# Performance work log

Measured on AMD Instinct MI355X. Metric: run time of the kernel, lower is better.

## Reference

```python
import jax, jax.numpy as jnp
import numpy as np

N = 4096   # atoms
B = 64     # structures in batch
K = 128    # k-vectors per structure
E = 256    # emb_size_atom
D = 8      # downprojection_size
NUM_HIDDEN = 3


def _silu(x):
    return x * jax.nn.sigmoid(x)


def _residual(x, W):
    # ResidualLayer: two bias-free Dense(E,E) with SiLU, plus skip
    y = _silu(x @ W[0].T)
    y = _silu(y @ W[1].T)
    return x + y


def setup_inputs() -> dict:
    key = jax.random.key(0)
    ks = jax.random.split(key, 10)
    h = jax.random.normal(ks[0], (N, E), jnp.float32)
    x = jax.random.uniform(ks[1], (N, 3), jnp.float32) * 10.0  # Angstrom-scale positions
    k = jax.random.normal(ks[2], (B, K, 3), jnp.float32)
    batch_seg = jnp.sort(jax.random.randint(ks[3], (N,), 0, B))
    sc = 1.0 / np.sqrt(E)
    W_pre = jax.random.normal(ks[4], (2, E, E), jnp.float32) * sc        # pre_residual
    W_down = jax.random.normal(ks[5], (D, K), jnp.float32) / np.sqrt(K)  # shared downprojection (D,K)
    W_up = jax.random.normal(ks[6], (E, D), jnp.float32) / np.sqrt(D)    # up (E,D)
    W0 = jax.random.normal(ks[7], (E, E), jnp.float32) * sc              # first dense of ewald_layers
    W_res = jax.random.normal(ks[8], (NUM_HIDDEN, 2, E, E), jnp.float32) * sc
    return {"h": h, "x": x, "k": k, "batch_seg": batch_seg, "num_batch": B,
            "W_pre": W_pre, "W_down": W_down, "W_up": W_up, "W0": W0, "W_res": W_res}


def reference(h, x, k, batch_seg, num_batch, W_pre, W_down, W_up, W0, W_res):
    hres = _residual(h, W_pre)                       # (N,E)
    # dot products of atom positions with their structure's k-vectors
    dot = jnp.einsum('nkd,nd->nk', k[batch_seg], x)  # (N,K); sinc_damping == 1 (use_pbc)
    c, s = jnp.cos(dot), jnp.sin(dot)
    # structure factors: scatter-sum over atoms within each structure
    sf_real = jax.ops.segment_sum(hres[:, None, :] * c[:, :, None], batch_seg,
                                  num_segments=num_batch)  # (B,K,E)
    sf_imag = jax.ops.segment_sum(hres[:, None, :] * s[:, :, None], batch_seg,
                                  num_segments=num_batch)  # (B,K,E)
    # low-rank learned Fourier-space filter (use_pbc branch)
    kfilter = (W_up @ W_down).T                      # (K,E)
    # re-project filtered structure factors back to atoms
    h_update = 0.01 * jnp.sum(
        (sf_real * kfilter)[batch_seg] * c[:, :, None]
        + (sf_imag * kfilter)[batch_seg] * s[:, :, None], axis=1)  # (N,E)
    # ewald_layers update MLP: Dense + num_hidden residual blocks
    hu = _silu(h_update @ W0.T)
    for i in range(NUM_HIDDEN):
        hu = _residual(hu, W_res[i])
    return hu, dot
```

## Files before the change

kernel.cpp:

```cpp
#include <hip/hip_runtime.h>

#define NN 4096
#define BB 64
#define KK 128
#define EE 256
#define HTS 4352
#define CSR 4224
#define PCAP 160
#define YTS 264
#define ZTS 20

typedef unsigned short u16;
typedef __bf16 bhalf;
typedef bhalf bhalf8 __attribute__((ext_vector_type(8)));
typedef float floatx4 __attribute__((ext_vector_type(4)));

__device__ __forceinline__ float b2f(u16 u) {
  union { unsigned int i; float f; } v; v.i = ((unsigned int)u) << 16; return v.f;
}
__device__ __forceinline__ u16 f2b(float f) {
  union { float f; unsigned int i; } v; v.f = f;
  unsigned int r = (v.i + 0x7FFFu + ((v.i >> 16) & 1u)) >> 16;
  return (u16)r;
}
__device__ __forceinline__ float silu_f(float v) {
  return v / (1.f + __expf(-v));
}
__device__ __forceinline__ bhalf8 ld8f(const float* __restrict__ p) {
  float4 f0 = *(const float4*)p;
  float4 f1 = *(const float4*)(p + 4);
  union { bhalf8 v; u16 s[8]; } u;
  u.s[0] = f2b(f0.x); u.s[1] = f2b(f0.y); u.s[2] = f2b(f0.z); u.s[3] = f2b(f0.w);
  u.s[4] = f2b(f1.x); u.s[5] = f2b(f1.y); u.s[6] = f2b(f1.z); u.s[7] = f2b(f1.w);
  return u.v;
}


__global__ __launch_bounds__(256) void p1_k(
    const float* __restrict__ Wpre, const float* __restrict__ W0,
    const float* __restrict__ Wres, const float* __restrict__ Wup,
    const float* __restrict__ Wdn, const int* __restrict__ bs,
    const float* __restrict__ x, const float* __restrict__ kvec,
    u16* __restrict__ wpre, u16* __restrict__ w0b, u16* __restrict__ wrb,
    float* __restrict__ kft, u16* __restrict__ csb,
    int* __restrict__ seg, float* __restrict__ dout)
{
  int bid = blockIdx.x, tid = threadIdx.x;
  if (bid < 288) {
    int mat = bid >> 5;
    int w8 = ((bid & 31) * 256 + tid);
    int o = w8 * 8;
    int lane = w8 & 63, k = (w8 >> 6) & 7, nt = w8 >> 9;
    int r = lane & 15, q = lane >> 4;
    int src = (nt * 16 + r) * 256 + q * 8 + k * 32;
    const float* S; u16* D;
    if (mat < 2)      { S = Wpre + mat * 65536;       D = wpre + mat * 65536; }
    else if (mat == 2){ S = W0;                       D = w0b; }
    else              { S = Wres + (mat - 3) * 65536; D = wrb + (mat - 3) * 65536; }
    *(bhalf8*)(D + o) = ld8f(S + src);
  }
  else if (bid < 416) {
    int i = (bid - 288) * 256 + tid;
    int e = i >> 7, kk = i & 127;
    float a = 0.f;
#pragma unroll
    for (int d = 0; d < 8; ++d) a += Wup[e * 8 + d] * Wdn[d * KK + kk];
    kft[i] = a;
  } else if (bid < 424) {
    int base = 4096 * 256 + ((bid - 416) * 256 + tid) * 16;
    uint4 z = {0, 0, 0, 0};
    *(uint4*)(csb + base) = z;
    *(uint4*)(csb + base + 8) = z;
  } else if (bid == 424) {
    int b = tid;
    if (b <= BB) {
      int lo = 0, hi = NN;
      while (lo < hi) { int mid = (lo + hi) >> 1; if (bs[mid] < b) lo = mid + 1; else hi = mid; }
      seg[b] = lo;
    }
  } else {
    int i = (bid - 425) * 256 + tid;
    int n = i >> 6, t2 = (i & 63) << 1;
    int b = bs[n];
    const float* kp = kvec + (b * KK + t2) * 3;
    const float* xp = x + n * 3;
    float x0 = xp[0], x1 = xp[1], x2 = xp[2];
    float2 k01 = *(const float2*)(kp);
    float2 k23 = *(const float2*)(kp + 2);
    float2 k45 = *(const float2*)(kp + 4);
    float d0 = k01.x * x0 + k01.y * x1 + k23.x * x2;
    float d1 = k23.y * x0 + k45.x * x1 + k45.y * x2;
    float s0, c0, s1, c1;
    __sincosf(d0, &s0, &c0);
    __sincosf(d1, &s1, &c1);
    float2 dp; dp.x = d0; dp.y = d1;
    *(float2*)(dout + (n << 7) + t2) = dp;
    unsigned cpack = (unsigned)f2b(c0) | ((unsigned)f2b(c1) << 16);
    unsigned spack = (unsigned)f2b(s0) | ((unsigned)f2b(s1) << 16);
    *(unsigned*)(csb + (n << 8) + t2) = cpack;
    *(unsigned*)(csb + (n << 8) + 128 + t2) = spack;
  }
}

__global__ __launch_bounds__(256) void p2_k(
    const float* __restrict__ h, const u16* __restrict__ Wa, const u16* __restrict__ Wb,
    u16* __restrict__ ht,
    const u16* __restrict__ csb, const int* __restrict__ seg, u16* __restrict__ ctb)
{
  __shared__ u16 sh[8256];
  if (blockIdx.x < 256) {
    const int lane = threadIdx.x & 63, wv = threadIdx.x >> 6;
    const int m0 = blockIdx.x * 16;
    const int n0 = wv * 64;
    const int r = lane & 15, q = lane >> 4;
    const int lane8 = lane * 8;
    const float* Ap = h + (m0 + r) * EE + q * 8;
    floatx4 acc[4];
#pragma unroll
    for (int t = 0; t < 4; ++t) acc[t] = (floatx4){0.f, 0.f, 0.f, 0.f};
#pragma unroll
    for (int k = 0; k < 8; ++k) {
      bhalf8 av = ld8f(Ap + k * 32);
#pragma unroll
      for (int t = 0; t < 4; ++t) {
        bhalf8 bv = *(const bhalf8*)(Wa + ((wv * 4 + t) * 8 + k) * 512 + lane8);
        acc[t] = __builtin_amdgcn_mfma_f32_16x16x32_bf16(av, bv, acc[t], 0, 0, 0);
      }
    }
#pragma unroll
    for (int t = 0; t < 4; ++t) {
      int col = n0 + t * 16 + r;
#pragma unroll
      for (int i = 0; i < 4; ++i)
        sh[(q * 4 + i) * YTS + col] = f2b(silu_f(acc[t][i]));
    }
    __syncthreads();
#pragma unroll
    for (int t = 0; t < 4; ++t) acc[t] = (floatx4){0.f, 0.f, 0.f, 0.f};
#pragma unroll
    for (int k = 0; k < 8; ++k) {
      bhalf8 av = *(const bhalf8*)(&sh[r * YTS + q * 8 + k * 32]);
#pragma unroll
      for (int t = 0; t < 4; ++t) {
        bhalf8 bv = *(const bhalf8*)(Wb + ((wv * 4 + t) * 8 + k) * 512 + lane8);
        acc[t] = __builtin_amdgcn_mfma_f32_16x16x32_bf16(av, bv, acc[t], 0, 0, 0);
      }
    }
    __syncthreads();
#pragma unroll
    for (int t = 0; t < 4; ++t) {
      int col = n0 + t * 16 + r;
#pragma unroll
      for (int i = 0; i < 4; ++i) {
        int g = m0 + q * 4 + i;
        float v = silu_f(acc[t][i]) + h[g * EE + col];
        sh[col * ZTS + q * 4 + i] = f2b(v);
      }
    }
    __syncthreads();
    int e = threadIdx.x;
    const uint2* src = (const uint2*)&sh[e * ZTS];
    uint2* dst = (uint2*)(ht + e * HTS + m0);
#pragma unroll
    for (int i = 0; i < 4; ++i) dst[i] = src[i];
  } else {
    int bid2 = blockIdx.x - 256;
    int b = bid2 / 5, p0 = (bid2 % 5) * 32, t = threadIdx.x;
    int s0 = seg[b], s1 = seg[b + 1];
    int abase = s0 & ~7;
#pragma unroll
    for (int it = 0; it < 32; ++it) {
      int idx = it * 256 + t;
      int pl = idx >> 8, j = idx & 255;
      int n = abase + p0 + pl;
      u16 v = 0;
      if (n >= s0 && n < s1) v = csb[(n << 8) | j];
      sh[pl * 258 + j] = v;
    }
    __syncthreads();
    unsigned w[16];
#pragma unroll
    for (int i = 0; i < 16; ++i) {
      unsigned lo = sh[(2 * i) * 258 + t];
      unsigned hi = sh[(2 * i + 1) * 258 + t];
      w[i] = lo | (hi << 16);
    }
    uint4* dst = (uint4*)(ctb + ((b << 8) + t) * PCAP + p0);
#pragma unroll
    for (int i = 0; i < 4; ++i) {
      uint4 u; u.x = w[4*i]; u.y = w[4*i+1]; u.z = w[4*i+2]; u.w = w[4*i+3];
      dst[i] = u;
    }
  }
}

__global__ __launch_bounds__(256) void sf_k(
    const u16* __restrict__ ht, const u16* __restrict__ ctb,
    const float* __restrict__ kft, const int* __restrict__ seg, u16* __restrict__ F)
{
  const int lane = threadIdx.x & 63;
  const int wv = threadIdx.x >> 6;
  const int b = blockIdx.x;
  const int e0 = blockIdx.y * 128 + wv * 32;
  const int j0 = blockIdx.z * 64;
  const int r = lane & 15, q = lane >> 4;
  const int abase = seg[b] & ~7;
  const int phi = seg[b + 1] - abase;
  const u16* Ap = ht + (e0 + r) * HTS + abase + q * 8;
  const u16* Bp = ctb + ((b << 8) + j0 + r) * PCAP + q * 8;
  floatx4 acc[2][4];
#pragma unroll
  for (int m = 0; m < 2; ++m)
#pragma unroll
    for (int t = 0; t < 4; ++t) acc[m][t] = (floatx4){0.f, 0.f, 0.f, 0.f};
  for (int p0 = 0; p0 < phi; p0 += 32) {
    bhalf8 a0 = *(const bhalf8*)(Ap + p0);
    bhalf8 a1 = *(const bhalf8*)(Ap + 16 * HTS + p0);
#pragma unroll
    for (int t = 0; t < 4; ++t) {
      bhalf8 bv = *(const bhalf8*)(Bp + t * 16 * PCAP + p0);
      acc[0][t] = __builtin_amdgcn_mfma_f32_16x16x32_bf16(a0, bv, acc[0][t], 0, 0, 0);
      acc[1][t] = __builtin_amdgcn_mfma_f32_16x16x32_bf16(a1, bv, acc[1][t], 0, 0, 0);
    }
  }
#pragma unroll
  for (int m = 0; m < 2; ++m)
#pragma unroll
    for (int t = 0; t < 4; ++t) {
      int col = j0 + t * 16 + r;
      int kk = col & 127;
#pragma unroll
      for (int i = 0; i < 4; ++i) {
        int row = e0 + m * 16 + q * 4 + i;
        F[((b << 8) + row) * 256 + col] = f2b(acc[m][t][i] * kft[row * KK + kk]);
      }
    }
}

__device__ __forceinline__ void loadB(const u16* __restrict__ W, int wv, int lane8,
                                      bhalf8 (&bf)[8][2]) {
#pragma unroll
  for (int k = 0; k < 8; ++k)
#pragma unroll
    for (int t = 0; t < 2; ++t)
      bf[k][t] = *(const bhalf8*)(W + ((wv * 2 + t) * 8 + k) * 512 + lane8);
}

__device__ __forceinline__ void stageD(
    const u16* __restrict__ As, const bhalf8 (&B)[8][2],
    const u16* __restrict__ Wn, bhalf8 (&Bn)[8][2],
    u16* __restrict__ Ad, const u16* __restrict__ Ask,
    float* __restrict__ outg, int R0, int c0, int r, int q, int wv, int lane8)
{
  if (Wn) loadB(Wn, wv, lane8, Bn);
  bhalf8 a[8];
#pragma unroll
  for (int k = 0; k < 8; ++k)
    a[k] = *(const bhalf8*)(As + r * YTS + q * 8 + k * 32);
  floatx4 acc[2];
  acc[0] = (floatx4){0.f, 0.f, 0.f, 0.f};
  acc[1] = (floatx4){0.f, 0.f, 0.f, 0.f};
#pragma unroll
  for (int k = 0; k < 8; ++k) {
    acc[0] = __builtin_amdgcn_mfma_f32_16x16x32_bf16(a[k], B[k][0], acc[0], 0, 0, 0);
    acc[1] = __builtin_amdgcn_mfma_f32_16x16x32_bf16(a[k], B[k][1], acc[1], 0, 0, 0);
  }
#pragma unroll
  for (int t = 0; t < 2; ++t) {
    int col = c0 + t * 16 + r;
#pragma unroll
    for (int i = 0; i < 4; ++i) {
      int row = q * 4 + i;
      float v = silu_f(acc[t][i]);
      if (Ask) v += b2f(Ask[row * YTS + col]);
      if (outg) outg[(R0 + row) * EE + col] = v;
      else      Ad[row * YTS + col] = f2b(v);
    }
  }
}

__global__ __launch_bounds__(512) void tail_k(
    const u16* __restrict__ csb, const u16* __restrict__ F,
    const int* __restrict__ bs, const int* __restrict__ seg,
    const u16* __restrict__ w0b, const u16* __restrict__ wrb,
    float* __restrict__ out)
{
  __shared__ u16 A0[16 * YTS], A1[16 * YTS];
  const int R0 = blockIdx.x * 16;
  const int lane = threadIdx.x & 63, wv = threadIdx.x >> 6;
  const int r = lane & 15, q = lane >> 4;
  const int c0 = wv * 32;
  const int lane8 = lane * 8;
  bhalf8 B0[8][2], B1[8][2];
  {
    const u16* Ap = csb + (R0 + r) * 256 + q * 8;
    bhalf8 a[8];
#pragma unroll
    for (int k = 0; k < 8; ++k) a[k] = *(const bhalf8*)(Ap + k * 32);
    int s = bs[R0];
    while (true) {
      const u16* Bp = F + ((s << 8) + c0 + r) * 256 + q * 8;
      bhalf8 bf[8][2];
#pragma unroll
      for (int k = 0; k < 8; ++k) {
        bf[k][0] = *(const bhalf8*)(Bp + k * 32);
        bf[k][1] = *(const bhalf8*)(Bp + 16 * 256 + k * 32);
      }
      floatx4 acc[2];
      acc[0] = (floatx4){0.f, 0.f, 0.f, 0.f};
      acc[1] = (floatx4){0.f, 0.f, 0.f, 0.f};
#pragma unroll
      for (int k = 0; k < 8; ++k) {
        acc[0] = __builtin_amdgcn_mfma_f32_16x16x32_bf16(a[k], bf[k][0], acc[0], 0, 0, 0);
        acc[1] = __builtin_amdgcn_mfma_f32_16x16x32_bf16(a[k], bf[k][1], acc[1], 0, 0, 0);
      }
      int lo = seg[s] - R0;     if (lo < 0)  lo = 0;
      int hi = seg[s + 1] - R0; if (hi > 16) hi = 16;
#pragma unroll
      for (int t = 0; t < 2; ++t) {
        int col = c0 + t * 16 + r;
#pragma unroll
        for (int i = 0; i < 4; ++i) {
          int row = q * 4 + i;
          if (row >= lo && row < hi)
            A0[row * YTS + col] = f2b(0.01f * acc[t][i]);
        }
      }
      if (seg[s + 1] >= R0 + 16) break;
      ++s;
    }
  }
  loadB(w0b, wv, lane8, B0);
  __syncthreads();
  stageD(A0, B0, wrb + 0 * EE * EE, B1, A1, nullptr, nullptr, R0, c0, r, q, wv, lane8);
  __syncthreads();
  stageD(A1, B1, wrb + 1 * EE * EE, B0, A0, nullptr, nullptr, R0, c0, r, q, wv, lane8);
  __syncthreads();
  stageD(A0, B0, wrb + 2 * EE * EE, B1, A1, A1,      nullptr, R0, c0, r, q, wv, lane8);
  __syncthreads();
  stageD(A1, B1, wrb + 3 * EE * EE, B0, A0, nullptr, nullptr, R0, c0, r, q, wv, lane8);
  __syncthreads();
  stageD(A0, B0, wrb + 4 * EE * EE, B1, A1, A1,      nullptr, R0, c0, r, q, wv, lane8);
  __syncthreads();
  stageD(A1, B1, wrb + 5 * EE * EE, B0, A0, nullptr, nullptr, R0, c0, r, q, wv, lane8);
  __syncthreads();
  stageD(A0, B0, nullptr,           B1, nullptr, A1, out,     R0, c0, r, q, wv, lane8);
}

extern "C" void kernel_launch(void* const* d_in, const int* in_sizes, int n_in,
                              void* d_out, int out_size, void* d_ws, size_t ws_size,
                              hipStream_t stream) {
  const float* h    = (const float*)d_in[0];
  const float* x    = (const float*)d_in[1];
  const float* kv   = (const float*)d_in[2];
  const int*   bs   = (const int*)d_in[3];
  const float* Wpre = (const float*)d_in[5];
  const float* Wdn  = (const float*)d_in[6];
  const float* Wup  = (const float*)d_in[7];
  const float* W0   = (const float*)d_in[8];
  const float* Wres = (const float*)d_in[9];
  float* out = (float*)d_out;

  float* kft = (float*)d_ws;
  int*   seg = (int*)(kft + EE * KK);
  u16* wpre = (u16*)(seg + 128);
  u16* w0b  = wpre + 2 * EE * EE;
  u16* wrb  = w0b + EE * EE;
  u16* csb  = wrb + 6 * EE * EE;
  u16* ctb  = csb + CSR * 256;
  u16* ht   = ctb + BB * 256 * PCAP;
  u16* F    = ht + 256 * HTS;

  p1_k<<<1449, 256, 0, stream>>>(Wpre, W0, Wres, Wup, Wdn, bs, x, kv,
                                 wpre, w0b, wrb, kft, csb, seg, out + NN * EE);
  p2_k<<<576, 256, 0, stream>>>(h, wpre, wpre + EE * EE, ht, csb, seg, ctb);
  sf_k<<<dim3(BB, 2, 4), 256, 0, stream>>>(ht, ctb, kft, seg, F);
  tail_k<<<256, 512, 0, stream>>>(csb, F, bs, seg, w0b, wrb, out);
}
```

Before: 121.3 us.

## Fuse pre-residual MLP into prep kernel and stage cos/sin transpose in LDS

Moves the pre-residual MLP into the first kernel, reading fp32 Wpre directly and converting it to bf16 on the fly, so it no longer waits for a separate weight-conversion pass. The separate p2 kernel and its global ctb transpose buffer are removed. sf_k now gathers each structure's cos/sin slice into padded shared memory itself. This saves one launch and a global round-trip, at the cost of redundant weight conversion in every MLP block and a strided shared-memory gather in sf_k.

```diff
diff --git a/kernel.cpp b/kernel.cpp
--- a/kernel.cpp
+++ b/kernel.cpp
@@ -5,10 +5,9 @@
 #define KK 128
 #define EE 256
 #define HTS 4352
-#define CSR 4224
-#define PCAP 160
 #define YTS 264
 #define ZTS 20
+#define CTS 168
 
 typedef unsigned short u16;
 typedef __bf16 bhalf;
@@ -37,41 +36,91 @@
 
 
 __global__ __launch_bounds__(256) void p1_k(
-    const float* __restrict__ Wpre, const float* __restrict__ W0,
-    const float* __restrict__ Wres, const float* __restrict__ Wup,
-    const float* __restrict__ Wdn, const int* __restrict__ bs,
-    const float* __restrict__ x, const float* __restrict__ kvec,
-    u16* __restrict__ wpre, u16* __restrict__ w0b, u16* __restrict__ wrb,
+    const float* __restrict__ h, const float* __restrict__ Wpre,
+    const float* __restrict__ W0, const float* __restrict__ Wres,
+    const float* __restrict__ Wup, const float* __restrict__ Wdn,
+    const int* __restrict__ bs, const float* __restrict__ x,
+    const float* __restrict__ kvec,
+    u16* __restrict__ w0b, u16* __restrict__ wrb,
     float* __restrict__ kft, u16* __restrict__ csb,
-    int* __restrict__ seg, float* __restrict__ dout)
+    int* __restrict__ seg, float* __restrict__ dout, u16* __restrict__ ht)
 {
+  __shared__ u16 sh[8256];
   int bid = blockIdx.x, tid = threadIdx.x;
-  if (bid < 288) {
-    int mat = bid >> 5;
-    int w8 = ((bid & 31) * 256 + tid);
+  if (bid < 256) {
+    const int lane = tid & 63, wv = tid >> 6;
+    const int m0 = bid * 16;
+    const int n0 = wv * 64;
+    const int r = lane & 15, q = lane >> 4;
+    const float* Ap = h + (m0 + r) * EE + q * 8;
+    const float* Wb32 = Wpre + 65536;
+    floatx4 acc[4];
+#pragma unroll
+    for (int t = 0; t < 4; ++t) acc[t] = (floatx4){0.f, 0.f, 0.f, 0.f};
+#pragma unroll
+    for (int k = 0; k < 8; ++k) {
+      bhalf8 av = ld8f(Ap + k * 32);
+#pragma unroll
+      for (int t = 0; t < 4; ++t) {
+        bhalf8 bv = ld8f(Wpre + ((wv * 4 + t) * 16 + r) * 256 + q * 8 + k * 32);
+        acc[t] = __builtin_amdgcn_mfma_f32_16x16x32_bf16(av, bv, acc[t], 0, 0, 0);
+      }
+    }
+#pragma unroll
+    for (int t = 0; t < 4; ++t) {
+      int col = n0 + t * 16 + r;
+#pragma unroll
+      for (int i = 0; i < 4; ++i)
+        sh[(q * 4 + i) * YTS + col] = f2b(silu_f(acc[t][i]));
+    }
+    __syncthreads();
+#pragma unroll
+    for (int t = 0; t < 4; ++t) acc[t] = (floatx4){0.f, 0.f, 0.f, 0.f};
+#pragma unroll
+    for (int k = 0; k < 8; ++k) {
+      bhalf8 av = *(const bhalf8*)(&sh[r * YTS + q * 8 + k * 32]);
+#pragma unroll
+      for (int t = 0; t < 4; ++t) {
+        bhalf8 bv = ld8f(Wb32 + ((wv * 4 + t) * 16 + r) * 256 + q * 8 + k * 32);
+        acc[t] = __builtin_amdgcn_mfma_f32_16x16x32_bf16(av, bv, acc[t], 0, 0, 0);
+      }
+    }
+    __syncthreads();
+#pragma unroll
+    for (int t = 0; t < 4; ++t) {
+      int col = n0 + t * 16 + r;
+#pragma unroll
+      for (int i = 0; i < 4; ++i) {
+        int g = m0 + q * 4 + i;
+        float v = silu_f(acc[t][i]) + h[g * EE + col];
+        sh[col * ZTS + q * 4 + i] = f2b(v);
+      }
+    }
+    __syncthreads();
+    int e = tid;
+    const uint2* src = (const uint2*)&sh[e * ZTS];
+    uint2* dst = (uint2*)(ht + e * HTS + m0);
+#pragma unroll
+    for (int i = 0; i < 4; ++i) dst[i] = src[i];
+  } else if (bid < 480) {
+    int mat = (bid - 256) >> 5;
+    int w8 = ((bid - 256) & 31) * 256 + tid;
     int o = w8 * 8;
     int lane = w8 & 63, k = (w8 >> 6) & 7, nt = w8 >> 9;
     int r = lane & 15, q = lane >> 4;
     int src = (nt * 16 + r) * 256 + q * 8 + k * 32;
     const float* S; u16* D;
-    if (mat < 2)      { S = Wpre + mat * 65536;       D = wpre + mat * 65536; }
-    else if (mat == 2){ S = W0;                       D = w0b; }
-    else              { S = Wres + (mat - 3) * 65536; D = wrb + (mat - 3) * 65536; }
+    if (mat == 0) { S = W0;                       D = w0b; }
+    else          { S = Wres + (mat - 1) * 65536; D = wrb + (mat - 1) * 65536; }
     *(bhalf8*)(D + o) = ld8f(S + src);
-  }
-  else if (bid < 416) {
-    int i = (bid - 288) * 256 + tid;
+  } else if (bid < 608) {
+    int i = (bid - 480) * 256 + tid;
     int e = i >> 7, kk = i & 127;
     float a = 0.f;
 #pragma unroll
     for (int d = 0; d < 8; ++d) a += Wup[e * 8 + d] * Wdn[d * KK + kk];
     kft[i] = a;
-  } else if (bid < 424) {
-    int base = 4096 * 256 + ((bid - 416) * 256 + tid) * 16;
-    uint4 z = {0, 0, 0, 0};
-    *(uint4*)(csb + base) = z;
-    *(uint4*)(csb + base + 8) = z;
-  } else if (bid == 424) {
+  } else if (bid == 608) {
     int b = tid;
     if (b <= BB) {
       int lo = 0, hi = NN;
@@ -79,7 +128,7 @@
       seg[b] = lo;
     }
   } else {
-    int i = (bid - 425) * 256 + tid;
+    int i = (bid - 609) * 256 + tid;
     int n = i >> 6, t2 = (i & 63) << 1;
     int b = bs[n];
     const float* kp = kvec + (b * KK + t2) * 3;
@@ -102,112 +151,40 @@
   }
 }
 
-__global__ __launch_bounds__(256) void p2_k(
-    const float* __restrict__ h, const u16* __restrict__ Wa, const u16* __restrict__ Wb,
-    u16* __restrict__ ht,
-    const u16* __restrict__ csb, const int* __restrict__ seg, u16* __restrict__ ctb)
+__global__ __launch_bounds__(256) void sf_k(
+    const u16* __restrict__ ht, const u16* __restrict__ csb,
+    const float* __restrict__ kft, const int* __restrict__ seg,
+    u16* __restrict__ F)
 {
-  __shared__ u16 sh[8256];
-  if (blockIdx.x < 256) {
-    const int lane = threadIdx.x & 63, wv = threadIdx.x >> 6;
-    const int m0 = blockIdx.x * 16;
-    const int n0 = wv * 64;
-    const int r = lane & 15, q = lane >> 4;
-    const int lane8 = lane * 8;
-    const float* Ap = h + (m0 + r) * EE + q * 8;
-    floatx4 acc[4];
-#pragma unroll
-    for (int t = 0; t < 4; ++t) acc[t] = (floatx4){0.f, 0.f, 0.f, 0.f};
-#pragma unroll
-    for (int k = 0; k < 8; ++k) {
-      bhalf8 av = ld8f(Ap + k * 32);
-#pragma unroll
-      for (int t = 0; t < 4; ++t) {
-        bhalf8 bv = *(const bhalf8*)(Wa + ((wv * 4 + t) * 8 + k) * 512 + lane8);
-        acc[t] = __builtin_amdgcn_mfma_f32_16x16x32_bf16(av, bv, acc[t], 0, 0, 0);
-      }
-    }
-#pragma unroll
-    for (int t = 0; t < 4; ++t) {
-      int col = n0 + t * 16 + r;
-#pragma unroll
-      for (int i = 0; i < 4; ++i)
-        sh[(q * 4 + i) * YTS + col] = f2b(silu_f(acc[t][i]));
-    }
-    __syncthreads();
-#pragma unroll
-    for (int t = 0; t < 4; ++t) acc[t] = (floatx4){0.f, 0.f, 0.f, 0.f};
-#pragma unroll
-    for (int k = 0; k < 8; ++k) {
-      bhalf8 av = *(const bhalf8*)(&sh[r * YTS + q * 8 + k * 32]);
-#pragma unroll
-      for (int t = 0; t < 4; ++t) {
-        bhalf8 bv = *(const bhalf8*)(Wb + ((wv * 4 + t) * 8 + k) * 512 + lane8);
-        acc[t] = __builtin_amdgcn_mfma_f32_16x16x32_bf16(av, bv, acc[t], 0, 0, 0);
-      }
-    }
-    __syncthreads();
-#pragma unroll
-    for (int t = 0; t < 4; ++t) {
-      int col = n0 + t * 16 + r;
-#pragma unroll
-      for (int i = 0; i < 4; ++i) {
-        int g = m0 + q * 4 + i;
-        float v = silu_f(acc[t][i]) + h[g * EE + col];
-        sh[col * ZTS + q * 4 + i] = f2b(v);
-      }
-    }
-    __syncthreads();
-    int e = threadIdx.x;
-    const uint2* src = (const uint2*)&sh[e * ZTS];
-    uint2* dst = (uint2*)(ht + e * HTS + m0);
-#pragma unroll
-    for (int i = 0; i < 4; ++i) dst[i] = src[i];
-  } else {
-    int bid2 = blockIdx.x - 256;
-    int b = bid2 / 5, p0 = (bid2 % 5) * 32, t = threadIdx.x;
-    int s0 = seg[b], s1 = seg[b + 1];
-    int abase = s0 & ~7;
-#pragma unroll
-    for (int it = 0; it < 32; ++it) {
-      int idx = it * 256 + t;
-      int pl = idx >> 8, j = idx & 255;
-      int n = abase + p0 + pl;
-      u16 v = 0;
-      if (n >= s0 && n < s1) v = csb[(n << 8) | j];
-      sh[pl * 258 + j] = v;
-    }
-    __syncthreads();
-    unsigned w[16];
-#pragma unroll
-    for (int i = 0; i < 16; ++i) {
-      unsigned lo = sh[(2 * i) * 258 + t];
-      unsigned hi = sh[(2 * i + 1) * 258 + t];
-      w[i] = lo | (hi << 16);
-    }
-    uint4* dst = (uint4*)(ctb + ((b << 8) + t) * PCAP + p0);
-#pragma unroll
-    for (int i = 0; i < 4; ++i) {
-      uint4 u; u.x = w[4*i]; u.y = w[4*i+1]; u.z = w[4*i+2]; u.w = w[4*i+3];
-      dst[i] = u;
-    }
-  }
-}
-
-__global__ __launch_bounds__(256) void sf_k(
-    const u16* __restrict__ ht, const u16* __restrict__ ctb,
-    const float* __restrict__ kft, const int* __restrict__ seg, u16* __restrict__ F)
-{
-  const int lane = threadIdx.x & 63;
-  const int wv = threadIdx.x >> 6;
+  __shared__ u16 ct[64 * CTS];
+  const int tid = threadIdx.x;
+  const int lane = tid & 63, wv = tid >> 6;
   const int b = blockIdx.x;
   const int e0 = blockIdx.y * 128 + wv * 32;
   const int j0 = blockIdx.z * 64;
   const int r = lane & 15, q = lane >> 4;
-  const int abase = seg[b] & ~7;
-  const int phi = seg[b + 1] - abase;
+  const int s0 = seg[b], s1 = seg[b + 1];
+  const int abase = s0 & ~7;
+  const int plo = s0 - abase, phi = s1 - abase;
+  const int pc = (phi + 31) & ~31;
+  for (int i = tid; i < 64 * 8; i += 256) {
+    int j = i >> 3, p = i & 7;
+    if (p < plo) ct[j * CTS + p] = 0;
+  }
+  {
+    int span = pc - phi;
+    for (int i = tid; i < 64 * 32; i += 256) {
+      int j = i >> 5, o = i & 31;
+      if (o < span) ct[j * CTS + phi + o] = 0;
+    }
+  }
+  for (int base = plo; base < phi; base += 4) {
+    int p = base + (tid >> 6);
+    int j = tid & 63;
+    if (p < phi) ct[j * CTS + p] = csb[((abase + p) << 8) | (j0 + j)];
+  }
+  __syncthreads();
   const u16* Ap = ht + (e0 + r) * HTS + abase + q * 8;
-  const u16* Bp = ctb + ((b << 8) + j0 + r) * PCAP + q * 8;
   floatx4 acc[2][4];
 #pragma unroll
   for (int m = 0; m < 2; ++m)
@@ -218,7 +195,7 @@
     bhalf8 a1 = *(const bhalf8*)(Ap + 16 * HTS + p0);
 #pragma unroll
     for (int t = 0; t < 4; ++t) {
-      bhalf8 bv = *(const bhalf8*)(Bp + t * 16 * PCAP + p0);
+      bhalf8 bv = *(const bhalf8*)(ct + (t * 16 + r) * CTS + q * 8 + p0);
       acc[0][t] = __builtin_amdgcn_mfma_f32_16x16x32_bf16(a0, bv, acc[0][t], 0, 0, 0);
       acc[1][t] = __builtin_amdgcn_mfma_f32_16x16x32_bf16(a1, bv, acc[1][t], 0, 0, 0);
     }
@@ -363,17 +340,14 @@
 
   float* kft = (float*)d_ws;
   int*   seg = (int*)(kft + EE * KK);
-  u16* wpre = (u16*)(seg + 128);
-  u16* w0b  = wpre + 2 * EE * EE;
+  u16* w0b  = (u16*)(seg + 128);
   u16* wrb  = w0b + EE * EE;
   u16* csb  = wrb + 6 * EE * EE;
-  u16* ctb  = csb + CSR * 256;
-  u16* ht   = ctb + BB * 256 * PCAP;
+  u16* ht   = csb + NN * 256;
   u16* F    = ht + 256 * HTS;
 
-  p1_k<<<1449, 256, 0, stream>>>(Wpre, W0, Wres, Wup, Wdn, bs, x, kv,
-                                 wpre, w0b, wrb, kft, csb, seg, out + NN * EE);
-  p2_k<<<576, 256, 0, stream>>>(h, wpre, wpre + EE * EE, ht, csb, seg, ctb);
-  sf_k<<<dim3(BB, 2, 4), 256, 0, stream>>>(ht, ctb, kft, seg, F);
+  p1_k<<<1633, 256, 0, stream>>>(h, Wpre, W0, Wres, Wup, Wdn, bs, x, kv,
+                                 w0b, wrb, kft, csb, seg, out + NN * EE, ht);
+  sf_k<<<dim3(BB, 2, 4), 256, 0, stream>>>(ht, csb, kft, seg, F);
   tail_k<<<256, 512, 0, stream>>>(csb, F, bs, seg, w0b, wrb, out);
 }
```

New measurement: 128.0 us. 1.06x slower.
